# Performance work log

Hardware: AMD Instinct MI355X
Metric: run time of the kernel (lower is better)

## Reference

```python
import jax, jax.numpy as jnp
import numpy as np

B, L, H, N = 4, 4096, 1024, 16
EPS = 1e-6  # layer_norm_epsilon


def setup_inputs() -> dict:
    key = jax.random.key(0)
    ks = jax.random.split(key, 8)
    hidden_states = jax.random.normal(ks[0], (B, L, H), dtype=jnp.float32)
    attention_mask = jnp.ones((B, L), dtype=jnp.float32)
    norm_weight = jnp.ones((H,), dtype=jnp.float32)
    # S4D init: dt log-uniform in [1e-3, 1e-1]; S4D-Lin A init; random C, D
    dt_min, dt_max = 1e-3, 1e-1
    log_dt = jax.random.uniform(ks[1], (H,), dtype=jnp.float32) * (
        float(np.log(dt_max)) - float(np.log(dt_min))) + float(np.log(dt_min))
    log_A_real = jnp.log(0.5 * jnp.ones((H, N), dtype=jnp.float32))
    A_imag = jnp.broadcast_to(float(np.pi) * jnp.arange(N, dtype=jnp.float32), (H, N))
    C_real = jax.random.normal(ks[2], (H, N), dtype=jnp.float32) * (0.5 ** 0.5)
    C_imag = jax.random.normal(ks[3], (H, N), dtype=jnp.float32) * (0.5 ** 0.5)
    D = jax.random.normal(ks[4], (H,), dtype=jnp.float32)
    out_w = jax.random.normal(ks[5], (2 * H, H), dtype=jnp.float32) * 0.02  # 1x1 conv to 2H (GLU)
    out_b = jnp.zeros((2 * H,), dtype=jnp.float32)
    return dict(hidden_states=hidden_states, attention_mask=attention_mask,
                norm_weight=norm_weight, log_dt=log_dt, log_A_real=log_A_real,
                A_imag=A_imag, C_real=C_real, C_imag=C_imag, D=D,
                out_w=out_w, out_b=out_b)


def _s4d_kernel(log_dt, log_A_real, A_imag, C_real, C_imag, length):
    """Diagonal SSM convolution kernel k[h, l] (S4D ZOH discretization)."""
    dt = jnp.exp(log_dt)                                   # (H,)
    A = -jnp.exp(log_A_real) + 1j * A_imag                 # (H, N) complex64
    C = C_real + 1j * C_imag                               # (H, N)
    dtA = A * dt[:, None]                                  # (H, N)
    C_disc = C * (jnp.exp(dtA) - 1.0) / A                  # (H, N)
    vand = jnp.exp(dtA[:, :, None] * jnp.arange(length, dtype=jnp.float32))  # (H, N, L)
    k = 2.0 * jnp.einsum('hn,hnl->hl', C_disc, vand).real  # (H, L)
    return k.astype(jnp.float32)


def reference(hidden_states, attention_mask, norm_weight, log_dt, log_A_real,
              A_imag, C_real, C_imag, D, out_w, out_b):
    # LongT5LayerNorm: RMSNorm (no mean subtraction), variance in fp32
    var = jnp.mean(jnp.square(hidden_states.astype(jnp.float32)), axis=-1, keepdims=True)
    normed = hidden_states * jax.lax.rsqrt(var + EPS) * norm_weight  # (B, L, H)
    # mask padded positions, go to channel-major layout (B, H, L)
    u = (normed * attention_mask[..., None]).transpose(0, 2, 1)
    Lx = u.shape[-1]
    k = _s4d_kernel(log_dt, log_A_real, A_imag, C_real, C_imag, Lx)  # (H, L)
    # causal convolution via FFT of length 2L
    nfft = 2 * Lx
    k_f = jnp.fft.rfft(k, n=nfft)                 # (H, nfft//2+1)
    u_f = jnp.fft.rfft(u, n=nfft)                 # (B, H, nfft//2+1)
    y = jnp.fft.irfft(u_f * k_f, n=nfft)[..., :Lx]  # (B, H, L)
    y = y + u * D[:, None]                        # skip connection
    y = jax.nn.gelu(y, approximate=False)         # torch nn.GELU (exact)
    # output 1x1 conv to 2H, then GLU over the channel dim
    z = jnp.einsum('bhl,oh->bol', y, out_w) + out_b[:, None]
    a, b = jnp.split(z, 2, axis=1)
    ssm_out = (a * jax.nn.sigmoid(b)).transpose(0, 2, 1)  # (B, L, H)
    # residual + dropout (eval mode -> identity)
    return hidden_states + ssm_out
```

## Files before the change

kernel.cpp:

```cpp
#include <hip/hip_runtime.h>

#define B_   4
#define L_   4096
#define H_   1024
#define N_   16
#define CH_  64
#define NC_  (L_/CH_)
#define M_   (B_*L_)
#define O2_  (2*H_)
#define EPS_ 1e-6f

typedef __attribute__((ext_vector_type(4))) float  f32x4;
typedef __attribute__((ext_vector_type(8))) __bf16 bf16x8;

__device__ __forceinline__ unsigned short f2bf(float x) {
  union { float f; unsigned int u; } v; v.f = x;
  unsigned int r = v.u + 0x7FFFu + ((v.u >> 16) & 1u);
  return (unsigned short)(r >> 16);
}
__device__ __forceinline__ float bf2f(unsigned short x) {
  union { unsigned int u; float f; } v; v.u = ((unsigned int)x) << 16;
  return v.f;
}

__device__ __forceinline__ void async_copy16(const void* g, void* l) {
  __builtin_amdgcn_global_load_lds(
      (const __attribute__((address_space(1))) unsigned int*)g,
      (__attribute__((address_space(3))) unsigned int*)l, 16, 0, 0);
}

__global__ void k_prep(const float* __restrict__ log_dt,
                       const float* __restrict__ log_A_real,
                       const float* __restrict__ A_imag,
                       const float* __restrict__ C_real,
                       const float* __restrict__ C_imag,
                       const float* __restrict__ outw,
                       const float* __restrict__ outb,
                       float* __restrict__ wr,  float* __restrict__ wi,
                       float* __restrict__ c2r, float* __restrict__ c2i,
                       float* __restrict__ wpr, float* __restrict__ wpi,
                       unsigned short* __restrict__ Wbf,
                       float* __restrict__ bp) {
  int idx = blockIdx.x * 256 + threadIdx.x;
  int p = idx >> 10, hh = idx & (H_ - 1);
  size_t src = (size_t)((p >> 1) + (p & 1) * H_) * H_ + hh;
  Wbf[idx] = f2bf(outw[src]);
  if (idx < O2_) bp[idx] = outb[(idx >> 1) + (idx & 1) * H_];
  if (idx < H_ * N_) {
    int h = idx / N_, n = idx % N_;
    int hn = h * N_ + n;
    float dt  = expf(log_dt[h]);
    float Ar  = -expf(log_A_real[hn]);
    float Ai  = A_imag[hn];
    float dr  = Ar * dt, di = Ai * dt;
    float er  = expf(dr);
    float wrv = er * cosf(di), wiv = er * sinf(di);
    float e1r = wrv - 1.0f, e1i = wiv;
    float den = Ar * Ar + Ai * Ai;
    float qr  = (e1r * Ar + e1i * Ai) / den;
    float qi  = (e1i * Ar - e1r * Ai) / den;
    float Cr  = C_real[hn], Ci = C_imag[hn];
    float cdr = Cr * qr - Ci * qi;
    float cdi = Cr * qi + Ci * qr;
    float ep  = expf((float)CH_ * dr);
    int o = n * H_ + h;
    wr[o]  = wrv;  wi[o]  = wiv;
    c2r[o] = 2.0f * cdr; c2i[o] = 2.0f * cdi;
    wpr[o] = ep * cosf((float)CH_ * di);
    wpi[o] = ep * sinf((float)CH_ * di);
  }
}

__global__ __launch_bounds__(256) void k_scale(const float* __restrict__ hs,
                                               const float* __restrict__ mask,
                                               float* __restrict__ scale) {
  int m = blockIdx.x, tid = threadIdx.x;
  float4 v = reinterpret_cast<const float4*>(hs + (size_t)m * H_)[tid];
  float s = v.x * v.x + v.y * v.y + v.z * v.z + v.w * v.w;
  #pragma unroll
  for (int off = 32; off > 0; off >>= 1) s += __shfl_down(s, off, 64);
  __shared__ float ps[4];
  if ((tid & 63) == 0) ps[tid >> 6] = s;
  __syncthreads();
  if (tid == 0) {
    float var = (ps[0] + ps[1] + ps[2] + ps[3]) * (1.0f / H_);
    scale[m] = rsqrtf(var + EPS_) * mask[m];
  }
}

__global__ __launch_bounds__(256) void k_scan1(const float* __restrict__ hs,
                                               const float* __restrict__ nw,
                                               const float* __restrict__ scale,
                                               const float* __restrict__ wr_,
                                               const float* __restrict__ wi_,
                                               float* __restrict__ endr,
                                               float* __restrict__ endi,
                                               unsigned short* __restrict__ ubf) {
  int tid = threadIdx.x;
  int h = blockIdx.x * 256 + tid;
  int c = blockIdx.y, b = blockIdx.z;
  float wr[N_], wi[N_], xr[N_], xi[N_];
  #pragma unroll
  for (int n = 0; n < N_; n++) {
    wr[n] = wr_[n * H_ + h]; wi[n] = wi_[n * H_ + h];
    xr[n] = 0.f; xi[n] = 0.f;
  }
  float nwh = nw[h];
  int l0 = c * CH_;
  const float* scp = scale + (size_t)b * L_ + l0;
  const float* hp = hs + ((size_t)b * L_ + l0) * H_ + h;
  unsigned short* up = ubf + ((size_t)b * L_ + l0) * H_ + h;
  #pragma unroll 8
  for (int l = 0; l < CH_; l++) {
    float u = hp[(size_t)l * H_] * scp[l] * nwh;
    unsigned short ub = f2bf(u);
    up[(size_t)l * H_] = ub;
    u = bf2f(ub);
    #pragma unroll
    for (int n = 0; n < N_; n++) {
      float oxr = xr[n];
      xr[n] = fmaf(wr[n], oxr, fmaf(-wi[n], xi[n], u));
      xi[n] = fmaf(wr[n], xi[n], wi[n] * oxr);
    }
  }
  size_t base = (((size_t)b * NC_ + c) * N_) * H_ + h;
  #pragma unroll
  for (int n = 0; n < N_; n++) {
    endr[base + (size_t)n * H_] = xr[n];
    endi[base + (size_t)n * H_] = xi[n];
  }
}

__global__ __launch_bounds__(256) void k_carry(const float* __restrict__ wpr_,
                                               const float* __restrict__ wpi_,
                                               const float* __restrict__ endr,
                                               const float* __restrict__ endi,
                                               float* __restrict__ carr,
                                               float* __restrict__ cari) {
  int idx = blockIdx.x * 256 + threadIdx.x;
  int h = idx & (H_ - 1);
  int n = (idx >> 10) & (N_ - 1);
  int b = idx >> 14;
  float wprv = wpr_[n * H_ + h], wpiv = wpi_[n * H_ + h];
  float sr = 0.f, si = 0.f;
  size_t cstride = (size_t)N_ * H_;
  size_t base = ((size_t)b * NC_) * cstride + (size_t)n * H_ + h;
  for (int c = 0; c < NC_; c++, base += cstride) {
    carr[base] = sr; cari[base] = si;
    float er = endr[base], ei = endi[base];
    float osr = sr;
    sr = fmaf(wprv, osr,  fmaf(-wpiv, si, er));
    si = fmaf(wprv, si, fmaf(wpiv, osr, ei));
  }
}

__global__ __launch_bounds__(256) void k_scan2(const unsigned short* __restrict__ ubf,
                                               const float* __restrict__ wr_,
                                               const float* __restrict__ wi_,
                                               const float* __restrict__ c2r_,
                                               const float* __restrict__ c2i_,
                                               const float* __restrict__ Dp,
                                               const float* __restrict__ carr,
                                               const float* __restrict__ cari,
                                               unsigned short* __restrict__ ybf) {
  int tid = threadIdx.x;
  int h = blockIdx.x * 256 + tid;
  int c = blockIdx.y, b = blockIdx.z;
  float wr[N_], wi[N_], cr[N_], ci[N_], xr[N_], xi[N_];
  size_t base = (((size_t)b * NC_ + c) * N_) * H_ + h;
  #pragma unroll
  for (int n = 0; n < N_; n++) {
    wr[n] = wr_[n * H_ + h]; wi[n] = wi_[n * H_ + h];
    cr[n] = c2r_[n * H_ + h]; ci[n] = c2i_[n * H_ + h];
    xr[n] = carr[base + (size_t)n * H_];
    xi[n] = cari[base + (size_t)n * H_];
  }
  float Dh = Dp[h];
  int l0 = c * CH_;
  const unsigned short* up = ubf + ((size_t)b * L_ + l0) * H_ + h;
  unsigned short* yp = ybf + ((size_t)b * L_ + l0) * H_ + h;
  #pragma unroll 8
  for (int l = 0; l < CH_; l++) {
    float u = bf2f(up[(size_t)l * H_]);
    float yv = u * Dh;
    #pragma unroll
    for (int n = 0; n < N_; n++) {
      float oxr = xr[n];
      xr[n] = fmaf(wr[n], oxr, fmaf(-wi[n], xi[n], u));
      xi[n] = fmaf(wr[n], xi[n], wi[n] * oxr);
      yv = fmaf(cr[n], xr[n], yv);
      yv = fmaf(-ci[n], xi[n], yv);
    }
    float g = 0.5f * yv * (1.0f + erff(yv * 0.70710678118654752f));
    yp[(size_t)l * H_] = f2bf(g);
  }
}

#define BM 128
#define BN 128
#define BKG 64
#define GSTRIDE 68
__global__ __launch_bounds__(256) void k_gemm(const unsigned short* __restrict__ A,
                                              const unsigned short* __restrict__ Bw,
                                              const float* __restrict__ bp,
                                              const float* __restrict__ hs,
                                              float* __restrict__ out) {
  __shared__ __align__(16) char smem[BM * GSTRIDE * 4];
  unsigned short* As = (unsigned short*)smem;
  unsigned short* Bs = As + BM * BKG;
  float* gt = (float*)smem;
  const int tid  = threadIdx.x;
  const int lane = tid & 63;
  const int wave = tid >> 6;
  const int bn = blockIdx.x * BN;
  const int bm = blockIdx.y * BM;
  const int wm = (wave >> 1) * 64;
  const int wn = (wave & 1) * 64;
  const int K = H_;
  f32x4 acc[4][4];
  #pragma unroll
  for (int mi = 0; mi < 4; mi++)
    #pragma unroll
    for (int ni = 0; ni < 4; ni++) acc[mi][ni] = (f32x4){0.f, 0.f, 0.f, 0.f};

  int rr[4], cc[4];
  #pragma unroll
  for (int i = 0; i < 4; i++) {
    int g = i * 256 + tid;
    rr[i] = g >> 3;
    cc[i] = ((g & 7) ^ (rr[i] & 7)) * 8;
  }
  const int ar = lane & 15, kqi = lane >> 4;

  for (int k0 = 0; k0 < K; k0 += BKG) {
    #pragma unroll
    for (int i = 0; i < 4; i++)
      async_copy16(A + (size_t)(bm + rr[i]) * K + k0 + cc[i], &As[(i * 256 + tid) * 8]);
    #pragma unroll
    for (int i = 0; i < 4; i++)
      async_copy16(Bw + (size_t)(bn + rr[i]) * K + k0 + cc[i], &Bs[(i * 256 + tid) * 8]);
    __syncthreads();
    #pragma unroll
    for (int kh = 0; kh < 2; kh++) {
      bf16x8 af[4], bf[4];
      #pragma unroll
      for (int mi = 0; mi < 4; mi++) {
        int row = wm + mi * 16 + ar;
        af[mi] = *reinterpret_cast<const bf16x8*>(
            &As[row * BKG + (((kh * 4 + kqi) ^ (row & 7)) * 8)]);
      }
      #pragma unroll
      for (int ni = 0; ni < 4; ni++) {
        int row = wn + ni * 16 + ar;
        bf[ni] = *reinterpret_cast<const bf16x8*>(
            &Bs[row * BKG + (((kh * 4 + kqi) ^ (row & 7)) * 8)]);
      }
      #pragma unroll
      for (int mi = 0; mi < 4; mi++)
        #pragma unroll
        for (int ni = 0; ni < 4; ni++)
          acc[mi][ni] = __builtin_amdgcn_mfma_f32_16x16x32_bf16(af[mi], bf[ni], acc[mi][ni], 0, 0, 0);
    }
    __syncthreads();
  }

  const int c4 = tid & 15;
  const int rw = tid >> 4;
  const size_t obase = (size_t)bm * H_ + (bn >> 1);
  float4 hv[8];
  #pragma unroll
  for (int rep = 0; rep < 8; rep++) {
    int row = rep * 16 + rw;
    hv[rep] = *reinterpret_cast<const float4*>(&hs[obase + (size_t)row * H_ + c4 * 4]);
  }
  #pragma unroll
  for (int ni = 0; ni < 4; ni++) {
    int p  = wn + ni * 16 + (lane & 15);
    int pe = (bn + p) & ~1;
    float bA = bp[pe], bB = bp[pe + 1];
    int jl = p >> 1;
    #pragma unroll
    for (int mi = 0; mi < 4; mi++) {
      int row0 = wm + mi * 16 + (lane >> 4) * 4;
      #pragma unroll
      for (int r = 0; r < 4; r++) {
        float v = acc[mi][ni][r];
        float w = __shfl_xor(v, 1, 64);
        if (!(lane & 1))
          gt[(row0 + r) * GSTRIDE + jl] = (v + bA) / (1.0f + __expf(-(w + bB)));
      }
    }
  }
  __syncthreads();
  #pragma unroll
  for (int rep = 0; rep < 8; rep++) {
    int row = rep * 16 + rw;
    float4 g = *reinterpret_cast<const float4*>(&gt[row * GSTRIDE + c4 * 4]);
    size_t o = obase + (size_t)row * H_ + c4 * 4;
    float4 rv = {hv[rep].x + g.x, hv[rep].y + g.y, hv[rep].z + g.z, hv[rep].w + g.w};
    *reinterpret_cast<float4*>(&out[o]) = rv;
  }
}

extern "C" void kernel_launch(void* const* d_in, const int* in_sizes, int n_in,
                              void* d_out, int out_size, void* d_ws, size_t ws_size,
                              hipStream_t stream) {
  const float* hs    = (const float*)d_in[0];
  const float* mask  = (const float*)d_in[1];
  const float* nw    = (const float*)d_in[2];
  const float* ldt   = (const float*)d_in[3];
  const float* lar   = (const float*)d_in[4];
  const float* aim   = (const float*)d_in[5];
  const float* crl   = (const float*)d_in[6];
  const float* cim   = (const float*)d_in[7];
  const float* Dp    = (const float*)d_in[8];
  const float* outw  = (const float*)d_in[9];
  const float* outb  = (const float*)d_in[10];
  float* out = (float*)d_out;

  size_t off = 0;
  char* ws = (char*)d_ws;
  auto nxt = [&](size_t bytes) -> void* {
    void* p = ws + off; off += (bytes + 255) & ~(size_t)255; return p;
  };
  float* wr   = (float*)nxt(H_ * N_ * 4);
  float* wi   = (float*)nxt(H_ * N_ * 4);
  float* c2r  = (float*)nxt(H_ * N_ * 4);
  float* c2i  = (float*)nxt(H_ * N_ * 4);
  float* wpr  = (float*)nxt(H_ * N_ * 4);
  float* wpi  = (float*)nxt(H_ * N_ * 4);
  float* bpck = (float*)nxt(O2_ * 4);
  float* scale= (float*)nxt((size_t)M_ * 4);
  float* endr = (float*)nxt((size_t)B_ * NC_ * N_ * H_ * 4);
  float* endi = (float*)nxt((size_t)B_ * NC_ * N_ * H_ * 4);
  float* carr = (float*)nxt((size_t)B_ * NC_ * N_ * H_ * 4);
  float* cari = (float*)nxt((size_t)B_ * NC_ * N_ * H_ * 4);
  unsigned short* Wbf = (unsigned short*)nxt((size_t)O2_ * H_ * 2);
  unsigned short* ubf = (unsigned short*)nxt((size_t)M_ * H_ * 2);
  unsigned short* ybf = (unsigned short*)nxt((size_t)M_ * H_ * 2);

  k_prep<<<dim3(O2_ * H_ / 256), dim3(256), 0, stream>>>(ldt, lar, aim, crl, cim,
                                                         outw, outb,
                                                         wr, wi, c2r, c2i, wpr, wpi,
                                                         Wbf, bpck);
  k_scale<<<dim3(M_), dim3(256), 0, stream>>>(hs, mask, scale);
  k_scan1<<<dim3(H_ / 256, NC_, B_), dim3(256), 0, stream>>>(hs, nw, scale, wr, wi,
                                                             endr, endi, ubf);
  k_carry<<<dim3(B_ * N_ * H_ / 256), dim3(256), 0, stream>>>(wpr, wpi, endr, endi, carr, cari);
  k_scan2<<<dim3(H_ / 256, NC_, B_), dim3(256), 0, stream>>>(ubf, wr, wi, c2r, c2i,
                                                             Dp, carr, cari, ybf);
  k_gemm<<<dim3(O2_ / BN, M_ / BM), dim3(256), 0, stream>>>(ybf, Wbf, bpck, hs, out);
}
```

Baseline: 363.1 us.

## Restructure scan2 to loop modes outer with LDS-staged input and per-position accumulators

The chunk scan kernel now stages its 64x256 bf16 input tile in shared memory with async copies. It swaps the loop order so each of the 16 state modes is scanned over the chunk one at a time, accumulating into a 64-entry per-thread output array. This removes the 96 per-mode state/coefficient registers and the strided global loads inside the time loop, at the cost of a 64-float accumulator array and 16 re-reads of the LDS tile. The GEMM epilogue also defers the residual hidden_states loads until after the GLU tile is written, which shortens live ranges and register pressure.

```diff
diff --git a/kernel.cpp b/kernel.cpp
--- a/kernel.cpp
+++ b/kernel.cpp
@@ -163,34 +163,46 @@
                                                const float* __restrict__ carr,
                                                const float* __restrict__ cari,
                                                unsigned short* __restrict__ ybf) {
+  __shared__ __align__(16) unsigned short us[CH_ * 256];
   int tid = threadIdx.x;
-  int h = blockIdx.x * 256 + tid;
+  int hb = blockIdx.x;
   int c = blockIdx.y, b = blockIdx.z;
-  float wr[N_], wi[N_], cr[N_], ci[N_], xr[N_], xi[N_];
+  int h = hb * 256 + tid;
+  int l0 = c * CH_;
+  const unsigned short* usrc = ubf + ((size_t)b * L_ + l0) * H_ + hb * 256;
+  #pragma unroll
+  for (int i = 0; i < 8; i++) {
+    int g = i * 256 + tid;
+    int l = g >> 5, hq = (g & 31) * 8;
+    async_copy16(usrc + (size_t)l * H_ + hq, &us[g * 8]);
+  }
+  __syncthreads();
+
+  float yacc[CH_];
+  float Dh = Dp[h];
+  #pragma unroll
+  for (int l = 0; l < CH_; l++)
+    yacc[l] = Dh * bf2f(us[l * 256 + tid]);
+
   size_t base = (((size_t)b * NC_ + c) * N_) * H_ + h;
-  #pragma unroll
   for (int n = 0; n < N_; n++) {
-    wr[n] = wr_[n * H_ + h]; wi[n] = wi_[n * H_ + h];
-    cr[n] = c2r_[n * H_ + h]; ci[n] = c2i_[n * H_ + h];
-    xr[n] = carr[base + (size_t)n * H_];
-    xi[n] = cari[base + (size_t)n * H_];
-  }
-  float Dh = Dp[h];
-  int l0 = c * CH_;
-  const unsigned short* up = ubf + ((size_t)b * L_ + l0) * H_ + h;
+    float wrv = wr_[n * H_ + h],  wiv = wi_[n * H_ + h];
+    float crv = c2r_[n * H_ + h], civ = c2i_[n * H_ + h];
+    float xr = carr[base + (size_t)n * H_];
+    float xi = cari[base + (size_t)n * H_];
+    #pragma unroll
+    for (int l = 0; l < CH_; l++) {
+      float u = bf2f(us[l * 256 + tid]);
+      float oxr = xr;
+      xr = fmaf(wrv, oxr, fmaf(-wiv, xi, u));
+      xi = fmaf(wrv, xi, wiv * oxr);
+      yacc[l] = fmaf(crv, xr, fmaf(-civ, xi, yacc[l]));
+    }
+  }
   unsigned short* yp = ybf + ((size_t)b * L_ + l0) * H_ + h;
-  #pragma unroll 8
+  #pragma unroll
   for (int l = 0; l < CH_; l++) {
-    float u = bf2f(up[(size_t)l * H_]);
-    float yv = u * Dh;
-    #pragma unroll
-    for (int n = 0; n < N_; n++) {
-      float oxr = xr[n];
-      xr[n] = fmaf(wr[n], oxr, fmaf(-wi[n], xi[n], u));
-      xi[n] = fmaf(wr[n], xi[n], wi[n] * oxr);
-      yv = fmaf(cr[n], xr[n], yv);
-      yv = fmaf(-ci[n], xi[n], yv);
-    }
+    float yv = yacc[l];
     float g = 0.5f * yv * (1.0f + erff(yv * 0.70710678118654752f));
     yp[(size_t)l * H_] = f2bf(g);
   }
@@ -264,15 +276,6 @@
     __syncthreads();
   }
 
-  const int c4 = tid & 15;
-  const int rw = tid >> 4;
-  const size_t obase = (size_t)bm * H_ + (bn >> 1);
-  float4 hv[8];
-  #pragma unroll
-  for (int rep = 0; rep < 8; rep++) {
-    int row = rep * 16 + rw;
-    hv[rep] = *reinterpret_cast<const float4*>(&hs[obase + (size_t)row * H_ + c4 * 4]);
-  }
   #pragma unroll
   for (int ni = 0; ni < 4; ni++) {
     int p  = wn + ni * 16 + (lane & 15);
@@ -292,13 +295,19 @@
     }
   }
   __syncthreads();
-  #pragma unroll
-  for (int rep = 0; rep < 8; rep++) {
-    int row = rep * 16 + rw;
-    float4 g = *reinterpret_cast<const float4*>(&gt[row * GSTRIDE + c4 * 4]);
-    size_t o = obase + (size_t)row * H_ + c4 * 4;
-    float4 rv = {hv[rep].x + g.x, hv[rep].y + g.y, hv[rep].z + g.z, hv[rep].w + g.w};
-    *reinterpret_cast<float4*>(&out[o]) = rv;
+  {
+    const int c4 = tid & 15;
+    const int rw = tid >> 4;
+    const size_t obase = (size_t)bm * H_ + (bn >> 1);
+    #pragma unroll
+    for (int rep = 0; rep < 8; rep++) {
+      int row = rep * 16 + rw;
+      float4 g = *reinterpret_cast<const float4*>(&gt[row * GSTRIDE + c4 * 4]);
+      size_t o = obase + (size_t)row * H_ + c4 * 4;
+      float4 hv = *reinterpret_cast<const float4*>(&hs[o]);
+      float4 rv = {hv.x + g.x, hv.y + g.y, hv.z + g.z, hv.w + g.w};
+      *reinterpret_cast<float4*>(&out[o]) = rv;
+    }
   }
 }
 
```

Measured after the change: 357.0 us. Within noise of the previous version (-1.7%).
